# Kernel tuning notes

Measured on AMD Instinct MI355X. Metric: run time of the kernel, lower is better.

Reference implementation:

```python
import jax, jax.numpy as jnp
import numpy as np

B, C, N, T, Hd, L, F = 128, 8, 256, 64, 256, 2, 32  # batch, conv_channels, num_nodes(=hidden), obs_len, hidden, num_layers, filter_num


def setup_inputs() -> dict:
    key = jax.random.key(0)
    ks = jax.random.split(key, 20)
    s = 0.05
    f32 = jnp.float32
    return {
        "x": jax.random.normal(ks[0], (B, C, N, T), f32),
        "wst": jax.random.normal(ks[1], (C,), f32) * s,            # st_conv 1x1 weight
        "bst": jax.random.normal(ks[2], (1,), f32) * s,
        "Wh": jax.random.normal(ks[3], (Hd, N), f32) * s,           # hidden Linear
        "bh": jax.random.normal(ks[4], (Hd,), f32) * s,
        "Wih": jax.random.normal(ks[5], (4 * Hd, Hd), f32) * s,     # LSTM
        "Whh": jax.random.normal(ks[6], (4 * Hd, Hd), f32) * s,
        "bih": jax.random.normal(ks[7], (4 * Hd,), f32) * s,
        "bhh": jax.random.normal(ks[8], (4 * Hd,), f32) * s,
        "Wd": jax.random.normal(ks[9], (Hd, 2 * Hd), f32) * s,      # den Linear(2h->h)
        "bd": jax.random.normal(ks[10], (Hd,), f32) * s,
        "Wc": jax.random.normal(ks[11], (F, T), f32) * s,           # attention conv kernel (filter_num,1,obs_len,1) squeezed
        "bc": jax.random.normal(ks[12], (F,), f32) * s,
        "Wl1": jax.random.normal(ks[13], (F, 2 * Hd), f32) * s,     # attention linear1
        "bl1": jax.random.normal(ks[14], (F,), f32) * s,
        "Wl2": jax.random.normal(ks[15], (Hd, 2 * Hd + F), f32) * s,  # attention linear2
        "bl2": jax.random.normal(ks[16], (Hd,), f32) * s,
        "wend": jax.random.normal(ks[17], (C,), f32) * s,           # end_conv 1x1 weight
        "bend": jax.random.normal(ks[18], (C,), f32) * s,
    }


def _forward(x, wst, bst, Wh, bh, Wih, Whh, bih, bhh, Wd, bd, Wc, bc, Wl1, bl1, Wl2, bl2, wend, bend):
    b = x.shape[0]
    # st_conv (1x1 over channels) + relu, then (B, obs_len, num_nodes)
    y = jax.nn.relu(jnp.einsum("bcnt,c->bnt", x, wst) + bst[0])
    xcon = jax.nn.relu(jnp.einsum("bnt,hn->bth", y, Wh) + bh)  # (B, T, Hd)

    def lstm_cell(xt, ht, ct):
        g = xt @ Wih.T + bih + ht @ Whh.T + bhh
        i, f, gg, o = jnp.split(g, 4, axis=1)
        c2 = jax.nn.sigmoid(f) * ct + jax.nn.sigmoid(i) * jnp.tanh(gg)
        h2 = jax.nn.sigmoid(o) * jnp.tanh(c2)
        return h2, c2

    def attention(Hbuf, htt2):
        # Hbuf: (b, T, Hd); htt2: (b, 2Hd)
        w = htt2 @ Wl1.T + bl1                                   # (b, F)
        cv = jax.nn.relu(jnp.einsum("bto,ft->bof", Hbuf, Wc) + bc)  # (b, Hd, F)
        alpha = jax.nn.sigmoid(jnp.sum(cv * w[:, None, :], axis=2))  # (b, Hd)
        v = jnp.sum(alpha[:, :, None] * cv, axis=1)              # (b, F)
        return jax.nn.relu(jnp.concatenate([htt2, v], axis=1)) @ Wl2.T + bl2

    def step(carry, xt):
        ht, ct, attn_out, Hbuf = carry
        xi = xt
        new_ht = attn_out
        for _ in range(L):
            xd = jnp.concatenate([xi, attn_out], axis=1) @ Wd.T + bd
            ht, ct = lstm_cell(xd, ht, ct)
            htt2 = jnp.concatenate([ct, ht], axis=1)             # (b, 2Hd)
            new_ht = attention(Hbuf, htt2)                       # (b, Hd)
            output = jnp.concatenate([ht, new_ht], axis=1) @ Wd.T + bd
            Hbuf = jax.nn.relu(jnp.concatenate([Hbuf[:, 1:, :], output[:, None, :]], axis=1))
            attn_out = new_ht
            xi = output
        return (ht, ct, attn_out, Hbuf), new_ht

    z = jnp.zeros((b, Hd), x.dtype)
    carry0 = (z, z, z, jnp.zeros((b, T, Hd), x.dtype))
    _, res = jax.lax.scan(step, carry0, jnp.transpose(xcon, (1, 0, 2)))  # (T, b, Hd)
    r = jax.nn.relu(jnp.transpose(res, (1, 2, 0)))              # (b, Hd, T)
    # end_conv 1x1: (b, C, Hd, T)
    return r[:, None, :, :] * wend[None, :, None, None] + bend[None, :, None, None]


def reference(x, wst, bst, Wh, bh, Wih, Whh, bih, bhh, Wd, bd, Wc, bc, Wl1, bl1, Wl2, bl2, wend, bend):
    return _forward(x, wst, bst, Wh, bh, Wih, Whh, bih, bhh, Wd, bd, Wc, bc, Wl1, bl1, Wl2, bl2, wend, bend)
```

## Files before the change

kernel.cpp:

```cpp
#include <hip/hip_runtime.h>
#include <hip/hip_bf16.h>

typedef unsigned int uint;
typedef unsigned short ushort;
typedef __fp16 half2_t __attribute__((ext_vector_type(2)));

__device__ __forceinline__ ushort f16b(float x){
  return __builtin_bit_cast(ushort, (_Float16)x);
}
__device__ __forceinline__ uint pk_rne(float a, float b){
  return (uint)f16b(a) | ((uint)f16b(b) << 16);
}
__device__ __forceinline__ void pk_hl(float a, float b, uint& h, uint& l){
  _Float16 ha = (_Float16)a, hb = (_Float16)b;
  float la = (a - (float)ha) * 2048.f;
  float lb = (b - (float)hb) * 2048.f;
  h = (uint)__builtin_bit_cast(ushort, ha) | ((uint)__builtin_bit_cast(ushort, hb) << 16);
  l = pk_rne(la, lb);
}
__device__ __forceinline__ float fdot2(uint a, uint b, float c){
#if __has_builtin(__builtin_amdgcn_fdot2)
  return __builtin_amdgcn_fdot2(__builtin_bit_cast(half2_t, a),
                                __builtin_bit_cast(half2_t, b), c, false);
#else
  half2_t ha = __builtin_bit_cast(half2_t, a), hb = __builtin_bit_cast(half2_t, b);
  return c + (float)ha.x*(float)hb.x + (float)ha.y*(float)hb.y;
#endif
}
__device__ __forceinline__ float sigm(float x){ return 1.0f/(1.0f+__expf(-x)); }
__device__ __forceinline__ float tanh_(float x){
  x = fminf(fmaxf(x, -15.f), 15.f);
  float e = __expf(-2.f*x);
  return (1.f-e)/(1.f+e);
}
#define LO_SCALE (1.0f/2048.0f)


__global__ void kPack(const float* __restrict__ Wd, const float* __restrict__ Wih,
                      const float* __restrict__ Whh, const float* __restrict__ Wl1,
                      const float* __restrict__ Wl2, const float* __restrict__ Wc,
                      const float* __restrict__ Wh,  const float* __restrict__ bih,
                      const float* __restrict__ bhh,
                      uint4* __restrict__ Wd4, uint4* __restrict__ Wc4hi,
                      uint4* __restrict__ Wc4lo, uint4* __restrict__ Wl24,
                      float* __restrict__ Wl1f, float* __restrict__ WcrotF,
                      uint* __restrict__ WhT2, float* __restrict__ bcomb)
{
  const int NTOT = 32768 + 65536 + 34816 + 16384 + 131072 + 32768 + 1024;
  for (int idx = blockIdx.x*blockDim.x + threadIdx.x; idx < NTOT; idx += gridDim.x*blockDim.x){
    int i = idx;
    if (i < 32768){
      int kpp=i>>8, o=i&255, k0=4*kpp;
      uint h0,l0,h1,l1;
      pk_hl(Wd[o*512+k0],   Wd[o*512+k0+1], h0,l0);
      pk_hl(Wd[o*512+k0+2], Wd[o*512+k0+3], h1,l1);
      Wd4[i] = make_uint4(h0,l0,h1,l1); continue; }
    i -= 32768;
    if (i < 65536){
      int kp=i>>8, hh=i&255;
      uint wh[4], wl[4];
      #pragma unroll
      for (int gi=0; gi<4; gi++){
        int row = gi*256+hh;
        float a,b;
        if (kp<128){ a=Wih[row*256+2*kp]; b=Wih[row*256+2*kp+1]; }
        else       { a=Whh[row*256+2*(kp-128)]; b=Whh[row*256+2*(kp-128)+1]; }
        pk_hl(a,b,wh[gi],wl[gi]);
      }
      Wc4hi[i] = make_uint4(wh[0],wh[1],wh[2],wh[3]);
      Wc4lo[i] = make_uint4(wl[0],wl[1],wl[2],wl[3]); continue; }
    i -= 65536;
    if (i < 34816){
      int kpp=i>>8, o=i&255, k0=4*kpp;
      uint h0,l0,h1,l1;
      pk_hl(Wl2[o*544+k0],   Wl2[o*544+k0+1], h0,l0);
      pk_hl(Wl2[o*544+k0+2], Wl2[o*544+k0+3], h1,l1);
      Wl24[i] = make_uint4(h0,l0,h1,l1); continue; }
    i -= 34816;
    if (i < 16384){ int kk=i>>5, f=i&31; Wl1f[i] = Wl1[f*512+kk]; continue; }
    i -= 16384;
    if (i < 131072){ int rb=i>>11, r=i&2047, s=r>>5, f=r&31;
      WcrotF[i] = Wc[f*64 + ((s - rb) & 63)]; continue; }
    i -= 131072;
    if (i < 32768){ int np=i>>8, h=i&255;
      WhT2[i] = pk_rne(Wh[h*256+2*np], Wh[h*256+2*np+1]); continue; }
    i -= 32768;
    bcomb[i] = bih[i] + bhh[i];
  }
}

__global__ void k1a(const float* __restrict__ x, const float* __restrict__ wst,
                    const float* __restrict__ bst, ushort* __restrict__ yT)
{
  int b = blockIdx.x, tq = blockIdx.y, n = threadIdx.x;
  float acc[16];
  #pragma unroll
  for (int k=0;k<16;k++) acc[k]=0.f;
  for (int c=0;c<8;c++){
    const float4* xp = (const float4*)(x + ((size_t)((b*8+c)*256 + n)*64 + tq*16));
    float wc = wst[c];
    #pragma unroll
    for (int q=0;q<4;q++){
      float4 v = xp[q];
      acc[4*q+0] += v.x*wc; acc[4*q+1] += v.y*wc;
      acc[4*q+2] += v.z*wc; acc[4*q+3] += v.w*wc;
    }
  }
  float b0 = bst[0];
  #pragma unroll
  for (int k=0;k<16;k++){
    float v = fmaxf(acc[k]+b0, 0.f);
    yT[(size_t)(b*64 + tq*16 + k)*256 + n] = f16b(v);
  }
}

__global__ void k1b(const uint* __restrict__ yT2, const uint* __restrict__ WhT2,
                    const float* __restrict__ bh, float* __restrict__ xcon)
{
  __shared__ uint yp[8192];
  int b = blockIdx.x, tid = threadIdx.x;
  for (int i = tid; i < 8192; i += 256) yp[i] = yT2[(size_t)b*8192 + i];
  __syncthreads();
  int h = tid;
  float bias = bh[h];
  for (int tq=0;tq<4;tq++){
    float acc[16];
    #pragma unroll
    for (int k=0;k<16;k++) acc[k]=0.f;
    for (int np=0;np<128;np++){
      uint w2 = WhT2[np*256 + h];
      #pragma unroll
      for (int k=0;k<16;k++)
        acc[k] = fdot2(yp[(tq*16+k)*128 + np], w2, acc[k]);
    }
    #pragma unroll
    for (int k=0;k<16;k++)
      xcon[(size_t)(b*64 + tq*16 + k)*256 + h] = fmaxf(acc[k]+bias, 0.f);
  }
}

__global__ __launch_bounds__(1024, 1)
void TPALSTM_17205638987874_kernel(const float* __restrict__ xcon,
        const uint4* __restrict__ Wd4, const uint4* __restrict__ Wc4hi,
        const uint4* __restrict__ Wc4lo, const uint4* __restrict__ Wl24,
        const float* __restrict__ Wl1f, const float* __restrict__ WcrotF,
        const float* __restrict__ bd, const float* __restrict__ bcomb,
        const float* __restrict__ bl1, const float* __restrict__ bl2,
        const float* __restrict__ bc, float* __restrict__ res)
{
  __shared__ float Hf32[64][256];
  __shared__ float cvs[256][33];
  __shared__ float gp[16][256];
  __shared__ float p4[4][256];
  __shared__ float ht[256], ct[256], alpha[256];
  __shared__ __align__(16) uint2 APR2[288];
  __shared__ float wv[32];

  int b = blockIdx.x, tid = threadIdx.x;
  int g = tid >> 8, o = tid & 255;
  int gu = __builtin_amdgcn_readfirstlane(g);

  for (int i = tid; i < 64*256; i += 1024) ((float*)Hf32)[i] = 0.f;
  if (tid < 256){ ht[tid]=0.f; ct[tid]=0.f; }
  if (tid >= 128 && tid < 256) APR2[tid] = make_uint2(0u,0u);
  if (tid < 128){
    const float* xr = xcon + (size_t)(b*64+0)*256;
    uint h,l; pk_hl(xr[2*tid], xr[2*tid+1], h, l);
    APR2[tid] = make_uint2(h,l);
  }
  __syncthreads();

  int base = 0;
  for (int t=0;t<64;t++){
    for (int l=0;l<2;l++){
      {
        float ahi=0.f, alo=0.f;
        const uint4* wp = Wd4 + (size_t)(g*32)*256 + o;
        const uint4* ap = (const uint4*)(APR2 + g*64);
        #pragma unroll 4
        for (int kpp=0;kpp<32;kpp++){
          uint4 w = wp[0]; wp += 256;
          uint4 A = ap[kpp];
          ahi = fdot2(A.x, w.x, ahi); alo = fdot2(A.y, w.x, alo); alo = fdot2(A.x, w.y, alo);
          ahi = fdot2(A.z, w.z, ahi); alo = fdot2(A.w, w.z, alo); alo = fdot2(A.z, w.w, alo);
        }
        p4[g][o] = ahi + alo*LO_SCALE;
      }
      __syncthreads();
      if (tid < 128){
        int o0=2*tid, o1=o0+1;
        float x0 = p4[0][o0]+p4[1][o0]+p4[2][o0]+p4[3][o0]+bd[o0];
        float x1 = p4[0][o1]+p4[1][o1]+p4[2][o1]+p4[3][o1]+bd[o1];
        uint h,l; pk_hl(x0,x1,h,l); APR2[tid]=make_uint2(h,l);
      } else if (tid < 256){
        int j=tid-128; uint h,l; pk_hl(ht[2*j], ht[2*j+1], h, l); APR2[tid]=make_uint2(h,l);
      }
      __syncthreads();
      {
        float ih=0.f,il=0.f,fh=0.f,fl=0.f,gh=0.f,gl=0.f,oh=0.f,ol=0.f;
        const uint4* whp = Wc4hi + (size_t)(g*64)*256 + o;
        const uint4* wlp = Wc4lo + (size_t)(g*64)*256 + o;
        #pragma unroll 4
        for (int kp=g*64; kp<g*64+64; kp++){
          uint4 w = whp[0]; whp += 256;
          uint4 v = wlp[0]; wlp += 256;
          uint2 A = APR2[kp];
          ih=fdot2(A.x,w.x,ih); il=fdot2(A.y,w.x,il); il=fdot2(A.x,v.x,il);
          fh=fdot2(A.x,w.y,fh); fl=fdot2(A.y,w.y,fl); fl=fdot2(A.x,v.y,fl);
          gh=fdot2(A.x,w.z,gh); gl=fdot2(A.y,w.z,gl); gl=fdot2(A.x,v.z,gl);
          oh=fdot2(A.x,w.w,oh); ol=fdot2(A.y,w.w,ol); ol=fdot2(A.x,v.w,ol);
        }
        gp[g*4+0][o]=ih+il*LO_SCALE; gp[g*4+1][o]=fh+fl*LO_SCALE;
        gp[g*4+2][o]=gh+gl*LO_SCALE; gp[g*4+3][o]=oh+ol*LO_SCALE;
      }
      __syncthreads();
      if (g==0){
        float gi = sigm (gp[0][o]+gp[4][o]+gp[8][o] +gp[12][o]+bcomb[o]);
        float gf = sigm (gp[1][o]+gp[5][o]+gp[9][o] +gp[13][o]+bcomb[256+o]);
        float gg = tanh_(gp[2][o]+gp[6][o]+gp[10][o]+gp[14][o]+bcomb[512+o]);
        float go = sigm (gp[3][o]+gp[7][o]+gp[11][o]+gp[15][o]+bcomb[768+o]);
        float c2 = gf*ct[o] + gi*gg;
        float h2 = go*tanh_(c2);
        ct[o]=c2; ht[o]=h2;
      }
      __syncthreads();
      if (tid < 128){ uint h,l; pk_hl(fmaxf(ct[2*tid],0.f), fmaxf(ct[2*tid+1],0.f), h,l); APR2[tid]=make_uint2(h,l); }
      else if (tid < 256){ int j=tid-128; uint h,l; pk_hl(fmaxf(ht[2*j],0.f), fmaxf(ht[2*j+1],0.f), h,l); APR2[tid]=make_uint2(h,l); }
      {
        int rb = base & 63;
        const float4* wp = (const float4*)(WcrotF + rb*2048 + gu*8);
        float a0=0.f,a1=0.f,a2=0.f,a3=0.f,a4=0.f,a5=0.f,a6=0.f,a7=0.f;
        #pragma unroll 4
        for (int s=0;s<64;s++){
          float hv = Hf32[s][o];
          float4 wa = wp[s*8];
          float4 wb = wp[s*8+1];
          a0 += hv*wa.x; a1 += hv*wa.y; a2 += hv*wa.z; a3 += hv*wa.w;
          a4 += hv*wb.x; a5 += hv*wb.y; a6 += hv*wb.z; a7 += hv*wb.w;
        }
        int f0 = gu*8;
        cvs[o][f0+0] = fmaxf(a0+bc[f0+0],0.f); cvs[o][f0+1] = fmaxf(a1+bc[f0+1],0.f);
        cvs[o][f0+2] = fmaxf(a2+bc[f0+2],0.f); cvs[o][f0+3] = fmaxf(a3+bc[f0+3],0.f);
        cvs[o][f0+4] = fmaxf(a4+bc[f0+4],0.f); cvs[o][f0+5] = fmaxf(a5+bc[f0+5],0.f);
        cvs[o][f0+6] = fmaxf(a6+bc[f0+6],0.f); cvs[o][f0+7] = fmaxf(a7+bc[f0+7],0.f);
      }
      if (g==3 && o < 32){
        int f = o;
        float a=0.f;
        const float* w = Wl1f + f;
        for (int k=0;k<256;k++) a += ct[k]*w[k*32];
        for (int k=0;k<256;k++) a += ht[k]*w[(256+k)*32];
        wv[f] = a + bl1[f];
      }
      __syncthreads();
      if (tid < 256){
        float s=0.f;
        #pragma unroll
        for (int f=0;f<32;f++) s += cvs[tid][f]*wv[f];
        alpha[tid] = sigm(s);
      }
      __syncthreads();
      if (tid < 256){
        int f = tid>>3, og = tid&7;
        float s=0.f;
        #pragma unroll 8
        for (int oo=0;oo<32;oo++){
          int oa = og*32+oo;
          s += alpha[oa]*cvs[oa][f];
        }
        s += __shfl_xor(s,1); s += __shfl_xor(s,2); s += __shfl_xor(s,4);
        float vn = __shfl_xor(s,8);
        if (og==0 && !(f&1)){
          uint h,l; pk_hl(fmaxf(s,0.f), fmaxf(vn,0.f), h,l);
          APR2[256+(f>>1)]=make_uint2(h,l);
        }
      }
      __syncthreads();
      {
        float ahi=0.f, alo=0.f;
        const uint4* wp = Wl24 + (size_t)(g*34)*256 + o;
        const uint4* ap = (const uint4*)(APR2 + g*68);
        #pragma unroll 4
        for (int kpp=0;kpp<34;kpp++){
          uint4 w = wp[0]; wp += 256;
          uint4 A = ap[kpp];
          ahi = fdot2(A.x, w.x, ahi); alo = fdot2(A.y, w.x, alo); alo = fdot2(A.x, w.y, alo);
          ahi = fdot2(A.z, w.z, ahi); alo = fdot2(A.w, w.z, alo); alo = fdot2(A.z, w.w, alo);
        }
        p4[g][o] = ahi + alo*LO_SCALE;
      }
      __syncthreads();
      if (tid<128){ uint h,l; pk_hl(ht[2*tid], ht[2*tid+1], h,l); APR2[tid]=make_uint2(h,l); }
      else if (tid<256){
        int j=tid-128, o0=2*j, o1=o0+1;
        float n0 = p4[0][o0]+p4[1][o0]+p4[2][o0]+p4[3][o0]+bl2[o0];
        float n1 = p4[0][o1]+p4[1][o1]+p4[2][o1]+p4[3][o1]+bl2[o1];
        uint h,l; pk_hl(n0,n1,h,l); APR2[tid]=make_uint2(h,l);
        alpha[o0] = n0; alpha[o1] = n1;
      }
      __syncthreads();
      if (l==1 && tid>=128 && tid<256){
        int j=tid-128, o0=2*j, o1=o0+1;
        float* rr = res + (size_t)(t*128+b)*256;
        rr[o0] = alpha[o0]; rr[o1] = alpha[o1];
      }
      {
        float ahi=0.f, alo=0.f;
        const uint4* wp = Wd4 + (size_t)(g*32)*256 + o;
        const uint4* ap = (const uint4*)(APR2 + g*64);
        #pragma unroll 4
        for (int kpp=0;kpp<32;kpp++){
          uint4 w = wp[0]; wp += 256;
          uint4 A = ap[kpp];
          ahi = fdot2(A.x, w.x, ahi); alo = fdot2(A.y, w.x, alo); alo = fdot2(A.x, w.y, alo);
          ahi = fdot2(A.z, w.z, ahi); alo = fdot2(A.w, w.z, alo); alo = fdot2(A.z, w.w, alo);
        }
        p4[g][o] = ahi + alo*LO_SCALE;
      }
      __syncthreads();
      if (tid<128){
        int o0=2*tid, o1=o0+1;
        float u0 = p4[0][o0]+p4[1][o0]+p4[2][o0]+p4[3][o0]+bd[o0];
        float u1 = p4[0][o1]+p4[1][o1]+p4[2][o1]+p4[3][o1]+bd[o1];
        int s = base & 63;
        Hf32[s][o0] = fmaxf(u0,0.f);
        Hf32[s][o1] = fmaxf(u1,0.f);
        if (l==0){
          uint h,lw; pk_hl(u0, u1, h, lw);
          APR2[tid]=make_uint2(h,lw);
        } else if (t < 63){
          const float* xr = xcon + (size_t)(b*64+t+1)*256;
          uint h,lw; pk_hl(xr[o0], xr[o1], h, lw);
          APR2[tid]=make_uint2(h,lw);
        }
      }
      __syncthreads();
      base++;
    }
  }
}

__global__ void k3(const float* __restrict__ res, const float* __restrict__ wend,
                   const float* __restrict__ bend, float* __restrict__ out)
{
  __shared__ float r2[64][257];
  int b = blockIdx.x, tid = threadIdx.x;
  for (int i = tid; i < 16384; i += 256){
    int t = i >> 8, h = i & 255;
    r2[t][h] = fmaxf(res[(size_t)(t*128+b)*256 + h], 0.f);
  }
  __syncthreads();
  int tt = tid & 63, hg = tid >> 6;
  for (int c=0;c<8;c++){
    float we = wend[c], be = bend[c];
    for (int hh=0;hh<64;hh++){
      int h = hg*64 + hh;
      out[((size_t)(b*8+c)*256 + h)*64 + tt] = r2[tt][h]*we + be;
    }
  }
}

extern "C" __attribute__((visibility("default"), used))
void kernel_launch(void* const* d_in, const int* in_sizes, int n_in,
                   void* d_out, int out_size, void* d_ws, size_t ws_size,
                   hipStream_t stream)
{
  const float* x    = (const float*)d_in[0];
  const float* wst  = (const float*)d_in[1];
  const float* bst  = (const float*)d_in[2];
  const float* Wh   = (const float*)d_in[3];
  const float* bh   = (const float*)d_in[4];
  const float* Wih  = (const float*)d_in[5];
  const float* Whh  = (const float*)d_in[6];
  const float* bih  = (const float*)d_in[7];
  const float* bhh  = (const float*)d_in[8];
  const float* Wd   = (const float*)d_in[9];
  const float* bd   = (const float*)d_in[10];
  const float* Wc   = (const float*)d_in[11];
  const float* bc   = (const float*)d_in[12];
  const float* Wl1  = (const float*)d_in[13];
  const float* bl1  = (const float*)d_in[14];
  const float* Wl2  = (const float*)d_in[15];
  const float* bl2  = (const float*)d_in[16];
  const float* wend = (const float*)d_in[17];
  const float* bend = (const float*)d_in[18];

  char* ws = (char*)d_ws;
  uint4* Wd4    = (uint4*)(ws + 0);
  uint4* Wc4hi  = (uint4*)(ws + 524288);
  uint4* Wc4lo  = (uint4*)(ws + 1572864);
  uint4* Wl24   = (uint4*)(ws + 2621440);
  float* Wl1f   = (float*)(ws + 3178496);
  float* WcrotF = (float*)(ws + 3244032);
  uint*  WhT2   = (uint*) (ws + 3768320);
  float* bcomb  = (float*)(ws + 3899392);
  ushort* yT    = (ushort*)(ws + 3903488);
  float* xcon   = (float*)(ws + 8097792);
  float* res    = (float*)(ws + 16486400);

  kPack<<<512, 256, 0, stream>>>(Wd, Wih, Whh, Wl1, Wl2, Wc, Wh, bih, bhh,
                                 Wd4, Wc4hi, Wc4lo, Wl24, Wl1f, WcrotF, WhT2, bcomb);
  k1a<<<dim3(128,4), 256, 0, stream>>>(x, wst, bst, yT);
  k1b<<<128, 256, 0, stream>>>((const uint*)yT, WhT2, bh, xcon);
  TPALSTM_17205638987874_kernel<<<128, 1024, 0, stream>>>(xcon, Wd4, Wc4hi, Wc4lo, Wl24,
                                                          Wl1f, WcrotF,
                                                          bd, bcomb, bl1, bl2, bc, res);
  k3<<<128, 256, 0, stream>>>(res, wend, bend, (float*)d_out);
}
```

Measured before the change: 4.988 ms.

## Keep first weight rows in registers, split Wl1 reduction, remap attention reads

Before the time loop, each thread loads the first two k-rows of the Wd, Wc hi/lo and Wl2 weight slices into registers. Every matvec then starts from these without waiting on global loads, which hides part of the load latency at the head of each loop. The Wl1 attention projection now uses 64 threads, with ct and ht halves summed by a shuffle. The alpha-weighted reduction reads cvs in an interleaved order, likely to cut LDS bank conflicts. The cost is 16 extra persistent uint4 registers per thread, which may lower occupancy or cause spills.

Measured after the change: 10.06 ms. 2.02x slower.

```diff
diff --git a/kernel.cpp b/kernel.cpp
--- a/kernel.cpp
+++ b/kernel.cpp
@@ -160,6 +160,15 @@
   int g = tid >> 8, o = tid & 255;
   int gu = __builtin_amdgcn_readfirstlane(g);
 
+  const uint4* s2base = Wd4  + (size_t)(g*32)*256 + o;
+  const uint4* s4hb   = Wc4hi + (size_t)(g*64)*256 + o;
+  const uint4* s4lb   = Wc4lo + (size_t)(g*64)*256 + o;
+  const uint4* s12b   = Wl24 + (size_t)(g*34)*256 + o;
+  uint4 pw0 = s2base[0],  pw1 = s2base[256];
+  uint4 ph0 = s4hb[0],    ph1 = s4hb[256];
+  uint4 pl0 = s4lb[0],    pl1 = s4lb[256];
+  uint4 pq0 = s12b[0],    pq1 = s12b[256];
+
   for (int i = tid; i < 64*256; i += 1024) ((float*)Hf32)[i] = 0.f;
   if (tid < 256){ ht[tid]=0.f; ct[tid]=0.f; }
   if (tid >= 128 && tid < 256) APR2[tid] = make_uint2(0u,0u);
@@ -175,10 +184,15 @@
     for (int l=0;l<2;l++){
       {
         float ahi=0.f, alo=0.f;
-        const uint4* wp = Wd4 + (size_t)(g*32)*256 + o;
         const uint4* ap = (const uint4*)(APR2 + g*64);
+        uint4 A0 = ap[0], A1 = ap[1];
+        ahi = fdot2(A0.x, pw0.x, ahi); alo = fdot2(A0.y, pw0.x, alo); alo = fdot2(A0.x, pw0.y, alo);
+        ahi = fdot2(A0.z, pw0.z, ahi); alo = fdot2(A0.w, pw0.z, alo); alo = fdot2(A0.z, pw0.w, alo);
+        ahi = fdot2(A1.x, pw1.x, ahi); alo = fdot2(A1.y, pw1.x, alo); alo = fdot2(A1.x, pw1.y, alo);
+        ahi = fdot2(A1.z, pw1.z, ahi); alo = fdot2(A1.w, pw1.z, alo); alo = fdot2(A1.z, pw1.w, alo);
+        const uint4* wp = s2base + 512;
         #pragma unroll 4
-        for (int kpp=0;kpp<32;kpp++){
+        for (int kpp=2;kpp<32;kpp++){
           uint4 w = wp[0]; wp += 256;
           uint4 A = ap[kpp];
           ahi = fdot2(A.x, w.x, ahi); alo = fdot2(A.y, w.x, alo); alo = fdot2(A.x, w.y, alo);
@@ -198,10 +212,24 @@
       __syncthreads();
       {
         float ih=0.f,il=0.f,fh=0.f,fl=0.f,gh=0.f,gl=0.f,oh=0.f,ol=0.f;
-        const uint4* whp = Wc4hi + (size_t)(g*64)*256 + o;
-        const uint4* wlp = Wc4lo + (size_t)(g*64)*256 + o;
+        {
+          uint2 A = APR2[g*64];
+          ih=fdot2(A.x,ph0.x,ih); il=fdot2(A.y,ph0.x,il); il=fdot2(A.x,pl0.x,il);
+          fh=fdot2(A.x,ph0.y,fh); fl=fdot2(A.y,ph0.y,fl); fl=fdot2(A.x,pl0.y,fl);
+          gh=fdot2(A.x,ph0.z,gh); gl=fdot2(A.y,ph0.z,gl); gl=fdot2(A.x,pl0.z,gl);
+          oh=fdot2(A.x,ph0.w,oh); ol=fdot2(A.y,ph0.w,ol); ol=fdot2(A.x,pl0.w,ol);
+        }
+        {
+          uint2 A = APR2[g*64+1];
+          ih=fdot2(A.x,ph1.x,ih); il=fdot2(A.y,ph1.x,il); il=fdot2(A.x,pl1.x,il);
+          fh=fdot2(A.x,ph1.y,fh); fl=fdot2(A.y,ph1.y,fl); fl=fdot2(A.x,pl1.y,fl);
+          gh=fdot2(A.x,ph1.z,gh); gl=fdot2(A.y,ph1.z,gl); gl=fdot2(A.x,pl1.z,gl);
+          oh=fdot2(A.x,ph1.w,oh); ol=fdot2(A.y,ph1.w,ol); ol=fdot2(A.x,pl1.w,ol);
+        }
+        const uint4* whp = s4hb + 512;
+        const uint4* wlp = s4lb + 512;
         #pragma unroll 4
-        for (int kp=g*64; kp<g*64+64; kp++){
+        for (int kp=g*64+2; kp<g*64+64; kp++){
           uint4 w = whp[0]; whp += 256;
           uint4 v = wlp[0]; wlp += 256;
           uint2 A = APR2[kp];
@@ -244,13 +272,14 @@
         cvs[o][f0+4] = fmaxf(a4+bc[f0+4],0.f); cvs[o][f0+5] = fmaxf(a5+bc[f0+5],0.f);
         cvs[o][f0+6] = fmaxf(a6+bc[f0+6],0.f); cvs[o][f0+7] = fmaxf(a7+bc[f0+7],0.f);
       }
-      if (g==3 && o < 32){
-        int f = o;
+      if (g==3 && o < 64){
+        int f = o & 31, kh = o >> 5;
         float a=0.f;
         const float* w = Wl1f + f;
-        for (int k=0;k<256;k++) a += ct[k]*w[k*32];
-        for (int k=0;k<256;k++) a += ht[k]*w[(256+k)*32];
-        wv[f] = a + bl1[f];
+        if (kh==0){ for (int k=0;k<256;k++) a += ct[k]*w[k*32]; }
+        else      { for (int k=0;k<256;k++) a += ht[k]*w[(256+k)*32]; }
+        a += __shfl_xor(a, 32);
+        if (kh==0) wv[f] = a + bl1[f];
       }
       __syncthreads();
       if (tid < 256){
@@ -265,7 +294,7 @@
         float s=0.f;
         #pragma unroll 8
         for (int oo=0;oo<32;oo++){
-          int oa = og*32+oo;
+          int oa = 4*og + (oo&3) + 32*(oo>>2);
           s += alpha[oa]*cvs[oa][f];
         }
         s += __shfl_xor(s,1); s += __shfl_xor(s,2); s += __shfl_xor(s,4);
@@ -278,10 +307,15 @@
       __syncthreads();
       {
         float ahi=0.f, alo=0.f;
-        const uint4* wp = Wl24 + (size_t)(g*34)*256 + o;
         const uint4* ap = (const uint4*)(APR2 + g*68);
+        uint4 A0 = ap[0], A1 = ap[1];
+        ahi = fdot2(A0.x, pq0.x, ahi); alo = fdot2(A0.y, pq0.x, alo); alo = fdot2(A0.x, pq0.y, alo);
+        ahi = fdot2(A0.z, pq0.z, ahi); alo = fdot2(A0.w, pq0.z, alo); alo = fdot2(A0.z, pq0.w, alo);
+        ahi = fdot2(A1.x, pq1.x, ahi); alo = fdot2(A1.y, pq1.x, alo); alo = fdot2(A1.x, pq1.y, alo);
+        ahi = fdot2(A1.z, pq1.z, ahi); alo = fdot2(A1.w, pq1.z, alo); alo = fdot2(A1.z, pq1.w, alo);
+        const uint4* wp = s12b + 512;
         #pragma unroll 4
-        for (int kpp=0;kpp<34;kpp++){
+        for (int kpp=2;kpp<34;kpp++){
           uint4 w = wp[0]; wp += 256;
           uint4 A = ap[kpp];
           ahi = fdot2(A.x, w.x, ahi); alo = fdot2(A.y, w.x, alo); alo = fdot2(A.x, w.y, alo);
@@ -306,10 +340,15 @@
       }
       {
         float ahi=0.f, alo=0.f;
-        const uint4* wp = Wd4 + (size_t)(g*32)*256 + o;
         const uint4* ap = (const uint4*)(APR2 + g*64);
+        uint4 A0 = ap[0], A1 = ap[1];
+        ahi = fdot2(A0.x, pw0.x, ahi); alo = fdot2(A0.y, pw0.x, alo); alo = fdot2(A0.x, pw0.y, alo);
+        ahi = fdot2(A0.z, pw0.z, ahi); alo = fdot2(A0.w, pw0.z, alo); alo = fdot2(A0.z, pw0.w, alo);
+        ahi = fdot2(A1.x, pw1.x, ahi); alo = fdot2(A1.y, pw1.x, alo); alo = fdot2(A1.x, pw1.y, alo);
+        ahi = fdot2(A1.z, pw1.z, ahi); alo = fdot2(A1.w, pw1.z, alo); alo = fdot2(A1.z, pw1.w, alo);
+        const uint4* wp = s2base + 512;
         #pragma unroll 4
-        for (int kpp=0;kpp<32;kpp++){
+        for (int kpp=2;kpp<32;kpp++){
           uint4 w = wp[0]; wp += 256;
           uint4 A = ap[kpp];
           ahi = fdot2(A.x, w.x, ahi); alo = fdot2(A.y, w.x, alo); alo = fdot2(A.x, w.y, alo);
```
